# Kernel optimization log

Measured on AMD Instinct MI355X. Metric: run time of the kernel, lower is better.

The kernel has to match this reference:

```python
import jax, jax.numpy as jnp
import numpy as np

B, T, D = 32, 4096, 512  # D = 2 * hidden_size


def setup_inputs() -> dict:
    key = jax.random.key(0)
    k_h, k_w1, k_b1, k_w2 = jax.random.split(key, 4)
    scale = 1.0 / np.sqrt(D)
    return {
        "hidden_states": jax.random.normal(k_h, (B, T, D), dtype=jnp.float32),
        "W1": jax.random.normal(k_w1, (D, D), dtype=jnp.float32) * scale,
        "b1": jax.random.normal(k_b1, (D,), dtype=jnp.float32) * scale,
        "W2": jax.random.normal(k_w2, (D, D), dtype=jnp.float32) * scale,
    }


def reference(hidden_states, W1, b1, W2):
    # u = tanh(h @ W1^T + b1)        [B, T, D]
    u = jnp.tanh(jnp.einsum("btd,ed->bte", hidden_states, W1) + b1)
    # alphas = softmax over time axis of u @ W2^T (no bias)   [B, T, D]
    alphas = jax.nn.softmax(jnp.einsum("btd,ed->bte", u, W2), axis=1)
    # Original loop cats weighted [T, D] slices along dim 0 then sums dim 0,
    # i.e. a global reduction over batch AND time -> [D]
    return jnp.sum(hidden_states * alphas, axis=(0, 1))
```

## Files before the change

### kernel.cpp

```cpp
#include <hip/hip_runtime.h>
#include <hip/hip_bf16.h>
#include <math.h>

#define BATCH 32
#define TLEN  4096
#define DDIM  512
#define BM    64
#define BLOCK 512

typedef __attribute__((ext_vector_type(8))) short bf16x8;
typedef __attribute__((ext_vector_type(4))) float f32x4;
typedef __attribute__((ext_vector_type(4))) short s16x4;

__device__ __forceinline__ short f32_to_bf16_rne(float f) {
    union { float f; unsigned int u; } v; v.f = f;
    unsigned int r = (v.u + 0x7FFFu + ((v.u >> 16) & 1u)) >> 16;
    return (short)r;
}
__device__ __forceinline__ float bf16_to_f32(short s) {
    union { unsigned int u; float f; } v;
    v.u = ((unsigned int)(unsigned short)s) << 16;
    return v.f;
}
__device__ __forceinline__ float fast_tanh(float x) {
    x = fminf(fmaxf(x, -15.f), 15.f);
    float t = __expf(2.0f * x);
    return (t - 1.0f) / (t + 1.0f);
}

__device__ __forceinline__ int lds_idx(int r, int c) {
    int g = (c >> 3) ^ (r & 31);
    return r * DDIM + (g << 3) + (c & 7);
}

__global__ void prep_kernel(const float* __restrict__ W1, const float* __restrict__ W2,
                            short* __restrict__ W1b, short* __restrict__ W2b,
                            float* __restrict__ lbuf, float* __restrict__ gbuf) {
    int i = blockIdx.x * blockDim.x + threadIdx.x;
    W1b[i] = f32_to_bf16_rne(W1[i]);
    W2b[i] = f32_to_bf16_rne(W2[i]);
    if (i < BATCH * DDIM) { lbuf[i] = 0.f; gbuf[i] = 0.f; }
}

__global__ __launch_bounds__(BLOCK, 2)
void main_kernel(const float* __restrict__ h,
                 const short* __restrict__ W1b,
                 const float* __restrict__ b1,
                 const short* __restrict__ W2b,
                 float* __restrict__ lbuf, float* __restrict__ gbuf) {
    __shared__ short sh[BM * DDIM];

    const int tid  = threadIdx.x;
    const int row0 = blockIdx.x * BM;
    const int b    = row0 / TLEN;

    {
        const float4* hp = (const float4*)(h + (size_t)row0 * DDIM);
        #pragma unroll
        for (int i = 0; i < (BM * DDIM / 4) / BLOCK; ++i) {
            int idx  = tid + i * BLOCK;
            float4 v = hp[idx];
            int flat = idx * 4;
            int r = flat >> 9;
            int c = flat & (DDIM - 1);
            s16x4 p;
            p.x = f32_to_bf16_rne(v.x); p.y = f32_to_bf16_rne(v.y);
            p.z = f32_to_bf16_rne(v.z); p.w = f32_to_bf16_rne(v.w);
            *(s16x4*)&sh[lds_idx(r, c)] = p;
        }
    }
    __syncthreads();

    const int wave = tid >> 6;
    const int lane = tid & 63;
    const int quad = lane >> 4;
    const int l16  = lane & 15;
    const int kq   = quad * 8;

    unsigned int u0pk[16];
    f32x4 acc[4][2];

    #pragma unroll
    for (int pass = 0; pass < 2; ++pass) {
        const int col0 = wave * 32 + pass * 256;
        #pragma unroll
        for (int rb = 0; rb < 4; ++rb)
            #pragma unroll
            for (int cb = 0; cb < 2; ++cb) acc[rb][cb] = (f32x4){0.f,0.f,0.f,0.f};

        const short* Bb = W1b + (size_t)(col0 + l16) * DDIM + kq;
        bf16x8 bcur[2], bnxt[2];
        #pragma unroll
        for (int cb = 0; cb < 2; ++cb)
            bcur[cb] = *(const bf16x8*)(Bb + cb * 16 * DDIM);

        for (int k0 = 0; k0 < DDIM; k0 += 32) {
            bf16x8 af[4];
            #pragma unroll
            for (int rb = 0; rb < 4; ++rb)
                af[rb] = *(const bf16x8*)&sh[lds_idx(rb * 16 + l16, k0 + kq)];
            #pragma unroll
            for (int cb = 0; cb < 2; ++cb)
                bnxt[cb] = *(const bf16x8*)(Bb + cb * 16 * DDIM + k0 + 32);
            #pragma unroll
            for (int cb = 0; cb < 2; ++cb)
                #pragma unroll
                for (int rb = 0; rb < 4; ++rb)
                    acc[rb][cb] = __builtin_amdgcn_mfma_f32_16x16x32_bf16(
                        af[rb], bcur[cb], acc[rb][cb], 0, 0, 0);
            #pragma unroll
            for (int cb = 0; cb < 2; ++cb) bcur[cb] = bnxt[cb];
        }

        #pragma unroll
        for (int cb = 0; cb < 2; ++cb) {
            float bias = b1[col0 + cb * 16 + l16];
            #pragma unroll
            for (int rb = 0; rb < 4; ++rb)
                #pragma unroll
                for (int r = 0; r < 4; ++r)
                    acc[rb][cb][r] = fast_tanh(acc[rb][cb][r] + bias);
        }
        if (pass == 0) {
            #pragma unroll
            for (int rb = 0; rb < 4; ++rb)
                #pragma unroll
                for (int r = 0; r < 4; ++r)
                    u0pk[rb * 4 + r] =
                        ((unsigned int)(unsigned short)f32_to_bf16_rne(acc[rb][0][r])) |
                        (((unsigned int)(unsigned short)f32_to_bf16_rne(acc[rb][1][r])) << 16);
        }
    }

    __syncthreads();

    #pragma unroll
    for (int cb = 0; cb < 2; ++cb) {
        int c0 = wave * 32 + cb * 16 + l16;
        int c1 = c0 + 256;
        #pragma unroll
        for (int rb = 0; rb < 4; ++rb)
            #pragma unroll
            for (int r = 0; r < 4; ++r) {
                int row = rb * 16 + quad * 4 + r;
                sh[lds_idx(row, c0)] = (short)(u0pk[rb * 4 + r] >> (cb * 16));
                sh[lds_idx(row, c1)] = f32_to_bf16_rne(acc[rb][cb][r]);
            }
    }
    __syncthreads();

    #pragma unroll
    for (int pass = 0; pass < 2; ++pass) {
        const int col0 = wave * 32 + pass * 256;
        #pragma unroll
        for (int rb = 0; rb < 4; ++rb)
            #pragma unroll
            for (int cb = 0; cb < 2; ++cb) acc[rb][cb] = (f32x4){0.f,0.f,0.f,0.f};

        const short* Bb = W2b + (size_t)(col0 + l16) * DDIM + kq;
        bf16x8 bcur[2], bnxt[2];
        #pragma unroll
        for (int cb = 0; cb < 2; ++cb)
            bcur[cb] = *(const bf16x8*)(Bb + cb * 16 * DDIM);

        for (int k0 = 0; k0 < DDIM; k0 += 32) {
            bf16x8 af[4];
            #pragma unroll
            for (int rb = 0; rb < 4; ++rb)
                af[rb] = *(const bf16x8*)&sh[lds_idx(rb * 16 + l16, k0 + kq)];
            #pragma unroll
            for (int cb = 0; cb < 2; ++cb)
                bnxt[cb] = *(const bf16x8*)(Bb + cb * 16 * DDIM + k0 + 32);
            #pragma unroll
            for (int cb = 0; cb < 2; ++cb)
                #pragma unroll
                for (int rb = 0; rb < 4; ++rb)
                    acc[rb][cb] = __builtin_amdgcn_mfma_f32_16x16x32_bf16(
                        af[rb], bcur[cb], acc[rb][cb], 0, 0, 0);
            #pragma unroll
            for (int cb = 0; cb < 2; ++cb) bcur[cb] = bnxt[cb];
        }

        #pragma unroll
        for (int cb = 0; cb < 2; ++cb) {
            int col = col0 + cb * 16 + l16;
            float hv[16];
            #pragma unroll
            for (int rb = 0; rb < 4; ++rb)
                #pragma unroll
                for (int r = 0; r < 4; ++r)
                    hv[rb * 4 + r] =
                        h[(size_t)(row0 + rb * 16 + quad * 4 + r) * DDIM + col];
            float lsum = 0.f, gsum = 0.f;
            #pragma unroll
            for (int rb = 0; rb < 4; ++rb)
                #pragma unroll
                for (int r = 0; r < 4; ++r) {
                    float e = __expf(acc[rb][cb][r]);
                    lsum += e;
                    gsum += e * hv[rb * 4 + r];
                }
            lsum += __shfl_xor(lsum, 16);  lsum += __shfl_xor(lsum, 32);
            gsum += __shfl_xor(gsum, 16);  gsum += __shfl_xor(gsum, 32);
            if (quad == 0) {
                atomicAdd(&lbuf[b * DDIM + col], lsum);
                atomicAdd(&gbuf[b * DDIM + col], gsum);
            }
        }
    }
}

__global__ void finish_kernel(const float* __restrict__ lbuf,
                              const float* __restrict__ gbuf,
                              float* __restrict__ out) {
    int d = blockIdx.x * blockDim.x + threadIdx.x;
    float s = 0.f;
    #pragma unroll
    for (int b = 0; b < BATCH; ++b)
        s += gbuf[b * DDIM + d] / lbuf[b * DDIM + d];
    out[d] = s;
}

extern "C" void kernel_launch(void* const* d_in, const int* in_sizes, int n_in,
                              void* d_out, int out_size, void* d_ws, size_t ws_size,
                              hipStream_t stream) {
    const float* h  = (const float*)d_in[0];
    const float* W1 = (const float*)d_in[1];
    const float* b1 = (const float*)d_in[2];
    const float* W2 = (const float*)d_in[3];
    float* out = (float*)d_out;

    char* ws = (char*)d_ws;
    short* W1b = (short*)ws;
    short* W2b = (short*)(ws + 512 * 1024);
    float* lbuf = (float*)(ws + 1024 * 1024);
    float* gbuf = (float*)(ws + 1024 * 1024 + 64 * 1024);

    prep_kernel<<<(DDIM * DDIM) / 256, 256, 0, stream>>>(W1, W2, W1b, W2b, lbuf, gbuf);
    main_kernel<<<(BATCH * TLEN) / BM, BLOCK, 0, stream>>>(h, W1b, b1, W2b, lbuf, gbuf);
    finish_kernel<<<2, 256, 0, stream>>>(lbuf, gbuf, out);
}
```

Measured before the change: 641.7 us.

## Use 32x32x16 MFMA with single-pass 64-column wave tiles for both GEMMs

Replaces the two-pass 16x16x32 MFMA tiling with 32x32x16 bf16 MFMA. Each wave now owns a contiguous 64-column slab of E, so each GEMM runs in a single pass over K instead of two. The first GEMM computes the transposed product (W1 as A operand) so tanh outputs can be written to LDS as packed 4-element stores, which removes the register stash of pass-0 results. This is meant to cut LDS re-reads of the activation tile and MFMA issue overhead, and to shorten the epilogue shuffle reduction, in exchange for larger accumulator register pressure.

```diff
diff --git a/kernel.cpp b/kernel.cpp
--- a/kernel.cpp
+++ b/kernel.cpp
@@ -1,5 +1,4 @@
 #include <hip/hip_runtime.h>
-#include <hip/hip_bf16.h>
 #include <math.h>
 
 #define BATCH 32
@@ -8,19 +7,14 @@
 #define BM    64
 #define BLOCK 512
 
-typedef __attribute__((ext_vector_type(8))) short bf16x8;
-typedef __attribute__((ext_vector_type(4))) float f32x4;
-typedef __attribute__((ext_vector_type(4))) short s16x4;
+typedef __attribute__((ext_vector_type(8)))  short bf16x8;
+typedef __attribute__((ext_vector_type(16))) float f32x16;
+typedef __attribute__((ext_vector_type(4)))  short s16x4;
 
 __device__ __forceinline__ short f32_to_bf16_rne(float f) {
     union { float f; unsigned int u; } v; v.f = f;
     unsigned int r = (v.u + 0x7FFFu + ((v.u >> 16) & 1u)) >> 16;
     return (short)r;
-}
-__device__ __forceinline__ float bf16_to_f32(short s) {
-    union { unsigned int u; float f; } v;
-    v.u = ((unsigned int)(unsigned short)s) << 16;
-    return v.f;
 }
 __device__ __forceinline__ float fast_tanh(float x) {
     x = fminf(fmaxf(x, -15.f), 15.f);
@@ -48,7 +42,7 @@
                  const float* __restrict__ b1,
                  const short* __restrict__ W2b,
                  float* __restrict__ lbuf, float* __restrict__ gbuf) {
-    __shared__ short sh[BM * DDIM];
+    __shared__ __align__(16) short sh[BM * DDIM];
 
     const int tid  = threadIdx.x;
     const int row0 = blockIdx.x * BM;
@@ -73,139 +67,150 @@
 
     const int wave = tid >> 6;
     const int lane = tid & 63;
-    const int quad = lane >> 4;
-    const int l16  = lane & 15;
-    const int kq   = quad * 8;
-
-    unsigned int u0pk[16];
-    f32x4 acc[4][2];
-
-    #pragma unroll
-    for (int pass = 0; pass < 2; ++pass) {
-        const int col0 = wave * 32 + pass * 256;
-        #pragma unroll
-        for (int rb = 0; rb < 4; ++rb)
-            #pragma unroll
-            for (int cb = 0; cb < 2; ++cb) acc[rb][cb] = (f32x4){0.f,0.f,0.f,0.f};
-
-        const short* Bb = W1b + (size_t)(col0 + l16) * DDIM + kq;
-        bf16x8 bcur[2], bnxt[2];
+    const int l32  = lane & 31;
+    const int h5   = lane >> 5;
+    const int e0   = wave * 64;
+
+    f32x16 acc[2][2];
+    #pragma unroll
+    for (int i = 0; i < 2; ++i)
+        #pragma unroll
+        for (int j = 0; j < 2; ++j)
+            #pragma unroll
+            for (int r = 0; r < 16; ++r) acc[i][j][r] = 0.f;
+
+    const short* W1p = W1b + (size_t)(e0 + l32) * DDIM + 8 * h5;
+    bf16x8 wc[2][2], wn[2][2];
+    #pragma unroll
+    for (int eb = 0; eb < 2; ++eb)
+        #pragma unroll
+        for (int ks = 0; ks < 2; ++ks)
+            wc[eb][ks] = *(const bf16x8*)(W1p + (size_t)eb * 32 * DDIM + ks * 16);
+
+    for (int k0 = 0; k0 < DDIM; k0 += 32) {
+        bf16x8 hf[2][2];
+        #pragma unroll
+        for (int tb = 0; tb < 2; ++tb)
+            #pragma unroll
+            for (int ks = 0; ks < 2; ++ks)
+                hf[tb][ks] = *(const bf16x8*)&sh[lds_idx(tb * 32 + l32,
+                                                         k0 + ks * 16 + 8 * h5)];
+        #pragma unroll
+        for (int eb = 0; eb < 2; ++eb)
+            #pragma unroll
+            for (int ks = 0; ks < 2; ++ks)
+                wn[eb][ks] = *(const bf16x8*)(W1p + (size_t)eb * 32 * DDIM
+                                              + k0 + 32 + ks * 16);
+        #pragma unroll
+        for (int eb = 0; eb < 2; ++eb)
+            #pragma unroll
+            for (int tb = 0; tb < 2; ++tb)
+                #pragma unroll
+                for (int ks = 0; ks < 2; ++ks)
+                    acc[eb][tb] = __builtin_amdgcn_mfma_f32_32x32x16_bf16(
+                        wc[eb][ks], hf[tb][ks], acc[eb][tb], 0, 0, 0);
+        #pragma unroll
+        for (int eb = 0; eb < 2; ++eb)
+            #pragma unroll
+            for (int ks = 0; ks < 2; ++ks) wc[eb][ks] = wn[eb][ks];
+    }
+
+    const short* W2p = W2b + (size_t)(e0 + l32) * DDIM + 8 * h5;
+    bf16x8 w2c[2][2], w2n[2][2];
+    #pragma unroll
+    for (int cb = 0; cb < 2; ++cb)
+        #pragma unroll
+        for (int ks = 0; ks < 2; ++ks)
+            w2c[cb][ks] = *(const bf16x8*)(W2p + (size_t)cb * 32 * DDIM + ks * 16);
+
+    #pragma unroll
+    for (int eb = 0; eb < 2; ++eb) {
+        float4 bv[4];
+        #pragma unroll
+        for (int q = 0; q < 4; ++q)
+            bv[q] = *(const float4*)&b1[e0 + 32 * eb + 4 * h5 + 8 * q];
+        #pragma unroll
+        for (int tb = 0; tb < 2; ++tb)
+            #pragma unroll
+            for (int r = 0; r < 16; ++r)
+                acc[eb][tb][r] = fast_tanh(acc[eb][tb][r] + bv[r >> 2][r & 3]);
+    }
+
+    __syncthreads();
+
+    #pragma unroll
+    for (int eb = 0; eb < 2; ++eb)
+        #pragma unroll
+        for (int tb = 0; tb < 2; ++tb) {
+            int t = tb * 32 + l32;
+            #pragma unroll
+            for (int q = 0; q < 4; ++q) {
+                int e = e0 + 32 * eb + 4 * h5 + 8 * q;
+                s16x4 p;
+                p.x = f32_to_bf16_rne(acc[eb][tb][4 * q + 0]);
+                p.y = f32_to_bf16_rne(acc[eb][tb][4 * q + 1]);
+                p.z = f32_to_bf16_rne(acc[eb][tb][4 * q + 2]);
+                p.w = f32_to_bf16_rne(acc[eb][tb][4 * q + 3]);
+                *(s16x4*)&sh[lds_idx(t, e)] = p;
+            }
+        }
+    __syncthreads();
+
+    f32x16 acc2[2][2];
+    #pragma unroll
+    for (int i = 0; i < 2; ++i)
+        #pragma unroll
+        for (int j = 0; j < 2; ++j)
+            #pragma unroll
+            for (int r = 0; r < 16; ++r) acc2[i][j][r] = 0.f;
+
+    for (int k0 = 0; k0 < DDIM; k0 += 32) {
+        bf16x8 uf[2][2];
+        #pragma unroll
+        for (int tb = 0; tb < 2; ++tb)
+            #pragma unroll
+            for (int ks = 0; ks < 2; ++ks)
+                uf[tb][ks] = *(const bf16x8*)&sh[lds_idx(tb * 32 + l32,
+                                                         k0 + ks * 16 + 8 * h5)];
         #pragma unroll
         for (int cb = 0; cb < 2; ++cb)
-            bcur[cb] = *(const bf16x8*)(Bb + cb * 16 * DDIM);
-
-        for (int k0 = 0; k0 < DDIM; k0 += 32) {
-            bf16x8 af[4];
-            #pragma unroll
-            for (int rb = 0; rb < 4; ++rb)
-                af[rb] = *(const bf16x8*)&sh[lds_idx(rb * 16 + l16, k0 + kq)];
-            #pragma unroll
-            for (int cb = 0; cb < 2; ++cb)
-                bnxt[cb] = *(const bf16x8*)(Bb + cb * 16 * DDIM + k0 + 32);
+            #pragma unroll
+            for (int ks = 0; ks < 2; ++ks)
+                w2n[cb][ks] = *(const bf16x8*)(W2p + (size_t)cb * 32 * DDIM
+                                               + k0 + 32 + ks * 16);
+        #pragma unroll
+        for (int tb = 0; tb < 2; ++tb)
             #pragma unroll
             for (int cb = 0; cb < 2; ++cb)
                 #pragma unroll
-                for (int rb = 0; rb < 4; ++rb)
-                    acc[rb][cb] = __builtin_amdgcn_mfma_f32_16x16x32_bf16(
-                        af[rb], bcur[cb], acc[rb][cb], 0, 0, 0);
-            #pragma unroll
-            for (int cb = 0; cb < 2; ++cb) bcur[cb] = bnxt[cb];
-        }
-
-        #pragma unroll
-        for (int cb = 0; cb < 2; ++cb) {
-            float bias = b1[col0 + cb * 16 + l16];
-            #pragma unroll
-            for (int rb = 0; rb < 4; ++rb)
-                #pragma unroll
-                for (int r = 0; r < 4; ++r)
-                    acc[rb][cb][r] = fast_tanh(acc[rb][cb][r] + bias);
-        }
-        if (pass == 0) {
-            #pragma unroll
-            for (int rb = 0; rb < 4; ++rb)
-                #pragma unroll
-                for (int r = 0; r < 4; ++r)
-                    u0pk[rb * 4 + r] =
-                        ((unsigned int)(unsigned short)f32_to_bf16_rne(acc[rb][0][r])) |
-                        (((unsigned int)(unsigned short)f32_to_bf16_rne(acc[rb][1][r])) << 16);
-        }
-    }
-
-    __syncthreads();
+                for (int ks = 0; ks < 2; ++ks)
+                    acc2[tb][cb] = __builtin_amdgcn_mfma_f32_32x32x16_bf16(
+                        uf[tb][ks], w2c[cb][ks], acc2[tb][cb], 0, 0, 0);
+        #pragma unroll
+        for (int cb = 0; cb < 2; ++cb)
+            #pragma unroll
+            for (int ks = 0; ks < 2; ++ks) w2c[cb][ks] = w2n[cb][ks];
+    }
 
     #pragma unroll
     for (int cb = 0; cb < 2; ++cb) {
-        int c0 = wave * 32 + cb * 16 + l16;
-        int c1 = c0 + 256;
-        #pragma unroll
-        for (int rb = 0; rb < 4; ++rb)
-            #pragma unroll
-            for (int r = 0; r < 4; ++r) {
-                int row = rb * 16 + quad * 4 + r;
-                sh[lds_idx(row, c0)] = (short)(u0pk[rb * 4 + r] >> (cb * 16));
-                sh[lds_idx(row, c1)] = f32_to_bf16_rne(acc[rb][cb][r]);
+        const int e2 = e0 + 32 * cb + l32;
+        const float* hp2 = h + (size_t)row0 * DDIM + e2;
+        float lsum = 0.f, gsum = 0.f;
+        #pragma unroll
+        for (int tb = 0; tb < 2; ++tb)
+            #pragma unroll
+            for (int r = 0; r < 16; ++r) {
+                int t = tb * 32 + 4 * h5 + (r & 3) + 8 * (r >> 2);
+                float ev = __expf(acc2[tb][cb][r]);
+                lsum += ev;
+                gsum += ev * hp2[(size_t)t * DDIM];
             }
-    }
-    __syncthreads();
-
-    #pragma unroll
-    for (int pass = 0; pass < 2; ++pass) {
-        const int col0 = wave * 32 + pass * 256;
-        #pragma unroll
-        for (int rb = 0; rb < 4; ++rb)
-            #pragma unroll
-            for (int cb = 0; cb < 2; ++cb) acc[rb][cb] = (f32x4){0.f,0.f,0.f,0.f};
-
-        const short* Bb = W2b + (size_t)(col0 + l16) * DDIM + kq;
-        bf16x8 bcur[2], bnxt[2];
-        #pragma unroll
-        for (int cb = 0; cb < 2; ++cb)
-            bcur[cb] = *(const bf16x8*)(Bb + cb * 16 * DDIM);
-
-        for (int k0 = 0; k0 < DDIM; k0 += 32) {
-            bf16x8 af[4];
-            #pragma unroll
-            for (int rb = 0; rb < 4; ++rb)
-                af[rb] = *(const bf16x8*)&sh[lds_idx(rb * 16 + l16, k0 + kq)];
-            #pragma unroll
-            for (int cb = 0; cb < 2; ++cb)
-                bnxt[cb] = *(const bf16x8*)(Bb + cb * 16 * DDIM + k0 + 32);
-            #pragma unroll
-            for (int cb = 0; cb < 2; ++cb)
-                #pragma unroll
-                for (int rb = 0; rb < 4; ++rb)
-                    acc[rb][cb] = __builtin_amdgcn_mfma_f32_16x16x32_bf16(
-                        af[rb], bcur[cb], acc[rb][cb], 0, 0, 0);
-            #pragma unroll
-            for (int cb = 0; cb < 2; ++cb) bcur[cb] = bnxt[cb];
-        }
-
-        #pragma unroll
-        for (int cb = 0; cb < 2; ++cb) {
-            int col = col0 + cb * 16 + l16;
-            float hv[16];
-            #pragma unroll
-            for (int rb = 0; rb < 4; ++rb)
-                #pragma unroll
-                for (int r = 0; r < 4; ++r)
-                    hv[rb * 4 + r] =
-                        h[(size_t)(row0 + rb * 16 + quad * 4 + r) * DDIM + col];
-            float lsum = 0.f, gsum = 0.f;
-            #pragma unroll
-            for (int rb = 0; rb < 4; ++rb)
-                #pragma unroll
-                for (int r = 0; r < 4; ++r) {
-                    float e = __expf(acc[rb][cb][r]);
-                    lsum += e;
-                    gsum += e * hv[rb * 4 + r];
-                }
-            lsum += __shfl_xor(lsum, 16);  lsum += __shfl_xor(lsum, 32);
-            gsum += __shfl_xor(gsum, 16);  gsum += __shfl_xor(gsum, 32);
-            if (quad == 0) {
-                atomicAdd(&lbuf[b * DDIM + col], lsum);
-                atomicAdd(&gbuf[b * DDIM + col], gsum);
-            }
+        lsum += __shfl_xor(lsum, 32);
+        gsum += __shfl_xor(gsum, 32);
+        if (h5 == 0) {
+            atomicAdd(&lbuf[b * DDIM + e2], lsum);
+            atomicAdd(&gbuf[b * DDIM + e2], gsum);
         }
     }
 }
```

Measured after the change: 643.2 us. No clear change (+0.2%).
